# Optimization experiments

Hardware: AMD Instinct MI355X
Metric: run time of the kernel (lower is better)

The kernel has to match this reference:

```python
import jax, jax.numpy as jnp
import numpy as np

EPS = 1e-5

def _ln(x, g, b):
    # layer norm over last dim
    m = jnp.mean(x, axis=-1, keepdims=True)
    v = jnp.mean((x - m) ** 2, axis=-1, keepdims=True)
    return (x - m) * jax.lax.rsqrt(v + EPS) * g + b

def setup_inputs() -> dict:
    key = jax.random.key(0)
    ks = jax.random.split(key, 12)
    B, T, E, H, OUT = 128, 256, 64, 128, 1
    GENOME = 1_000_000
    D = 2 * E  # input_size_lstm
    inp = {}
    inp["indices"] = jax.random.randint(ks[0], (B, T, 2), 0, GENOME, dtype=jnp.int64)
    inp["h0"] = jax.random.normal(ks[1], (B, H), dtype=jnp.float32)
    inp["c0"] = jax.random.normal(ks[2], (B, H), dtype=jnp.float32)
    inp["embed_table"] = jax.random.normal(ks[3], (GENOME, E), dtype=jnp.float32)
    s_ih = 1.0 / np.sqrt(D)
    s_hh = 1.0 / np.sqrt(H)
    inp["W_ih"] = jax.random.uniform(ks[4], (4 * H, D), minval=-s_ih, maxval=s_ih, dtype=jnp.float32)
    inp["W_hh"] = jax.random.uniform(ks[5], (4 * H, H), minval=-s_hh, maxval=s_hh, dtype=jnp.float32)
    inp["g_ih"] = jnp.ones((4 * H,), jnp.float32)
    inp["b_ih"] = jnp.zeros((4 * H,), jnp.float32)
    inp["g_hh"] = jnp.ones((4 * H,), jnp.float32)
    inp["b_hh"] = jnp.zeros((4 * H,), jnp.float32)
    inp["g_c"] = jnp.ones((H,), jnp.float32)
    inp["b_c"] = jnp.zeros((H,), jnp.float32)
    s_o = 1.0 / np.sqrt(H * T)
    inp["W_out"] = jax.random.uniform(ks[6], (OUT * T, H * T), minval=-s_o, maxval=s_o, dtype=jnp.float32)
    inp["b_out"] = jax.random.uniform(ks[7], (OUT * T,), minval=-s_o, maxval=s_o, dtype=jnp.float32)
    return inp

def _forward(indices, embed_table, W_ih, W_hh, g_ih, b_ih, g_hh, b_hh, g_c, b_c, W_out, b_out, h0, c0):
    B, T = indices.shape[0], indices.shape[1]
    H = h0.shape[-1]
    # embedding gather: (B,T,2,E) -> (B,T,2E)
    emb = embed_table[indices].reshape(B, T, -1)
    # precompute input-to-hidden gates for all timesteps: (B,T,4H)
    x_gates = jnp.einsum("btd,gd->btg", emb, W_ih)

    def step(carry, xg):
        h, c = carry
        gates = _ln(xg, g_ih, b_ih) + _ln(h @ W_hh.T, g_hh, b_hh)
        i, f, g, o = jnp.split(gates, 4, axis=-1)
        c_new = jax.nn.sigmoid(f) * c + jax.nn.sigmoid(i) * jnp.tanh(g)
        h_new = jax.nn.sigmoid(o) * jnp.tanh(_ln(c_new, g_c, b_c))
        return (h_new, c_new), h_new

    (_, _), hs = jax.lax.scan(step, (h0, c0), jnp.swapaxes(x_gates, 0, 1))
    # hs: (T,B,H) -> (B,T*H)
    seq_out = jnp.swapaxes(hs, 0, 1).reshape(B, T * H)
    out = jax.nn.sigmoid(seq_out @ W_out.T + b_out)
    return out, emb

def reference(indices, h0, c0, embed_table, W_ih, W_hh, g_ih, b_ih, g_hh, b_hh, g_c, b_c, W_out, b_out):
    return _forward(indices, embed_table, W_ih, W_hh, g_ih, b_ih, g_hh, b_hh, g_c, b_c, W_out, b_out, h0, c0)
```

## Files before the change

kernel.cpp:

```cpp
#include <hip/hip_runtime.h>
#include <cstddef>


typedef __attribute__((ext_vector_type(8))) _Float16 f16x8;
typedef __attribute__((ext_vector_type(4))) float f32x4;

__device__ __forceinline__ float frcp(float x) { return __builtin_amdgcn_rcpf(x); }
__device__ __forceinline__ float sigm(float x) { return frcp(1.0f + __expf(-x)); }
__device__ __forceinline__ float ftanh(float x) {
  float e = __expf(2.0f * x);
  return (e - 1.0f) * frcp(e + 1.0f);
}
__device__ __forceinline__ void split2(float x, unsigned short& hi, unsigned short& lo) {
  _Float16 h = (_Float16)x;
  _Float16 l = (_Float16)((x - (float)h) * 2048.0f);
  hi = *(unsigned short*)&h;
  lo = *(unsigned short*)&l;
}
__device__ __forceinline__ void barrier_lds() {
  asm volatile("s_waitcnt lgkmcnt(0)\n\ts_barrier" ::: "memory");
}

#define SEL4(v, jj) ((jj) == 0 ? (v)[0] : (jj) == 1 ? (v)[1] : (jj) == 2 ? (v)[2] : (v)[3])

__global__ void k_embed(const int* __restrict__ idx, const float4* __restrict__ table4,
                        float4* __restrict__ emb4) {
  int i = blockIdx.x * blockDim.x + threadIdx.x;
  int p = i >> 4, j = i & 15;
  int id = idx[p];
  emb4[(size_t)p * 16 + j] = table4[(size_t)id * 16 + j];
}

__global__ __launch_bounds__(256) void k_gemm_tn(
    const float* __restrict__ A, const float* __restrict__ Bm, float* __restrict__ C,
    int K, int kchunks, int N, size_t partstride)
{
  __shared__ float As[64][65];
  __shared__ float Bs[64][68];
  const int tid = threadIdx.x;
  const int tx = tid & 15, ty = tid >> 4;
  const int m0 = blockIdx.x * 64, n0 = blockIdx.y * 64;
  float acc[4][4] = {};
  size_t kbase = (size_t)blockIdx.z * kchunks * 64;
  for (int kc = 0; kc < kchunks; ++kc) {
    size_t k0 = kbase + (size_t)kc * 64;
    #pragma unroll
    for (int it = 0; it < 4; ++it) {
      int fi = it * 256 + tid;
      int row = fi >> 4, col4 = fi & 15;
      float4 va = *(const float4*)(A + (size_t)(m0 + row) * K + k0 + col4 * 4);
      As[row][col4*4+0] = va.x; As[row][col4*4+1] = va.y;
      As[row][col4*4+2] = va.z; As[row][col4*4+3] = va.w;
      float4 vb = *(const float4*)(Bm + (size_t)(n0 + row) * K + k0 + col4 * 4);
      Bs[col4*4+0][row] = vb.x; Bs[col4*4+1][row] = vb.y;
      Bs[col4*4+2][row] = vb.z; Bs[col4*4+3][row] = vb.w;
    }
    __syncthreads();
    #pragma unroll 8
    for (int k = 0; k < 64; ++k) {
      float a0 = As[ty*4+0][k], a1 = As[ty*4+1][k], a2 = As[ty*4+2][k], a3 = As[ty*4+3][k];
      float b0 = Bs[k][tx*4+0], b1 = Bs[k][tx*4+1], b2 = Bs[k][tx*4+2], b3 = Bs[k][tx*4+3];
      acc[0][0] += a0*b0; acc[0][1] += a0*b1; acc[0][2] += a0*b2; acc[0][3] += a0*b3;
      acc[1][0] += a1*b0; acc[1][1] += a1*b1; acc[1][2] += a1*b2; acc[1][3] += a1*b3;
      acc[2][0] += a2*b0; acc[2][1] += a2*b1; acc[2][2] += a2*b2; acc[2][3] += a2*b3;
      acc[3][0] += a3*b0; acc[3][1] += a3*b1; acc[3][2] += a3*b2; acc[3][3] += a3*b3;
    }
    __syncthreads();
  }
  float* Cp = C + (size_t)blockIdx.z * partstride;
  #pragma unroll
  for (int i = 0; i < 4; ++i) {
    float4 v = make_float4(acc[i][0], acc[i][1], acc[i][2], acc[i][3]);
    *(float4*)(Cp + (size_t)(m0 + ty*4 + i) * N + n0 + tx*4) = v;
  }
}

__global__ __launch_bounds__(256) void k_xln(float4* __restrict__ xg4,
                                             const float4* __restrict__ g4,
                                             const float4* __restrict__ bi4,
                                             const float4* __restrict__ bh4) {
  int row = blockIdx.x * 4 + (threadIdx.x >> 6);
  int lane = threadIdx.x & 63;
  float4* r = xg4 + (size_t)row * 128;
  float4 a = r[lane], b = r[lane + 64];
  float s = a.x + a.y + a.z + a.w + b.x + b.y + b.z + b.w;
  float q = a.x*a.x + a.y*a.y + a.z*a.z + a.w*a.w + b.x*b.x + b.y*b.y + b.z*b.z + b.w*b.w;
  #pragma unroll
  for (int off = 32; off; off >>= 1) { s += __shfl_xor(s, off); q += __shfl_xor(q, off); }
  float m = s * (1.0f / 512.0f);
  float rs = rsqrtf(q * (1.0f / 512.0f) - m * m + 1e-5f);
  float4 ga = g4[lane], gb = g4[64 + lane];
  float4 ia = bi4[lane], ib = bi4[64 + lane];
  float4 ha = bh4[lane], hb = bh4[64 + lane];
  a.x = (a.x - m) * rs * ga.x + ia.x + ha.x; a.y = (a.y - m) * rs * ga.y + ia.y + ha.y;
  a.z = (a.z - m) * rs * ga.z + ia.z + ha.z; a.w = (a.w - m) * rs * ga.w + ia.w + ha.w;
  b.x = (b.x - m) * rs * gb.x + ib.x + hb.x; b.y = (b.y - m) * rs * gb.y + ib.y + hb.y;
  b.z = (b.z - m) * rs * gb.z + ib.z + hb.z; b.w = (b.w - m) * rs * gb.w + ib.w + hb.w;
  r[lane] = a; r[lane + 64] = b;
}

__global__ void k_wprep(const float* __restrict__ Whh, uint4* __restrict__ wfh,
                        uint4* __restrict__ wfl) {
  int i = blockIdx.x * 256 + threadIdx.x;
  int l = i & 63, kc = (i >> 6) & 3, mt = i >> 8;
  int row = mt * 16 + (l & 15);
  int kb = kc * 32 + 8 * (l >> 4);
  float4 a = *(const float4*)(Whh + row * 128 + kb);
  float4 c = *(const float4*)(Whh + row * 128 + kb + 4);
  unsigned short h0,h1,h2,h3,h4,h5,h6,h7, l0,l1,l2,l3,l4,l5,l6,l7;
  split2(a.x,h0,l0); split2(a.y,h1,l1); split2(a.z,h2,l2); split2(a.w,h3,l3);
  split2(c.x,h4,l4); split2(c.y,h5,l5); split2(c.z,h6,l6); split2(c.w,h7,l7);
  uint4 oh, ol;
  oh.x = h0 | ((unsigned)h1 << 16); oh.y = h2 | ((unsigned)h3 << 16);
  oh.z = h4 | ((unsigned)h5 << 16); oh.w = h6 | ((unsigned)h7 << 16);
  ol.x = l0 | ((unsigned)l1 << 16); ol.y = l2 | ((unsigned)l3 << 16);
  ol.z = l4 | ((unsigned)l5 << 16); ol.w = l6 | ((unsigned)l7 << 16);
  wfh[i] = oh; wfl[i] = ol;
}

__global__ __launch_bounds__(512, 2) void k_scan(
    const float* __restrict__ xln,
    const uint4* __restrict__ wfh,
    const uint4* __restrict__ wfl,
    const float* __restrict__ h0, const float* __restrict__ c0,
    const float* __restrict__ g_hh,
    const float* __restrict__ g_c,  const float* __restrict__ b_c,
    float* __restrict__ hs)
{
  const int b = blockIdx.x;
  const int tid = threadIdx.x;
  const int w = tid >> 6, l = tid & 63;
  const int lg = l >> 4;
  const int jj = (l & 15) >> 2;
  const bool wr = (l & 3) == 0;
  const int u = w * 16 + lg * 4 + jj;
  const float inv2048 = 1.0f / 2048.0f;

  __shared__ alignas(16) unsigned short hbh[128];
  __shared__ alignas(16) unsigned short hbl[128];
  __shared__ float2 hred[8];
  __shared__ float2 cred[8];

  uint4 afh0[4], afh1[4], afh2[4], afh3[4];
  uint4 afl0[4], afl1[4], afl2[4], afl3[4];
  #pragma unroll
  for (int kc = 0; kc < 4; ++kc) {
    afh0[kc] = wfh[((w     ) * 4 + kc) * 64 + l];
    afh1[kc] = wfh[((w +  8) * 4 + kc) * 64 + l];
    afh2[kc] = wfh[((w + 16) * 4 + kc) * 64 + l];
    afh3[kc] = wfh[((w + 24) * 4 + kc) * 64 + l];
    afl0[kc] = wfl[((w     ) * 4 + kc) * 64 + l];
    afl1[kc] = wfl[((w +  8) * 4 + kc) * 64 + l];
    afl2[kc] = wfl[((w + 16) * 4 + kc) * 64 + l];
    afl3[kc] = wfl[((w + 24) * 4 + kc) * 64 + l];
  }
  #pragma unroll
  for (int kc = 0; kc < 4; ++kc) {
    asm volatile("" : "+v"(afh0[kc].x), "+v"(afh0[kc].y), "+v"(afh0[kc].z), "+v"(afh0[kc].w));
    asm volatile("" : "+v"(afh1[kc].x), "+v"(afh1[kc].y), "+v"(afh1[kc].z), "+v"(afh1[kc].w));
    asm volatile("" : "+v"(afh2[kc].x), "+v"(afh2[kc].y), "+v"(afh2[kc].z), "+v"(afh2[kc].w));
    asm volatile("" : "+v"(afh3[kc].x), "+v"(afh3[kc].y), "+v"(afh3[kc].z), "+v"(afh3[kc].w));
    asm volatile("" : "+v"(afl0[kc].x), "+v"(afl0[kc].y), "+v"(afl0[kc].z), "+v"(afl0[kc].w));
    asm volatile("" : "+v"(afl1[kc].x), "+v"(afl1[kc].y), "+v"(afl1[kc].z), "+v"(afl1[kc].w));
    asm volatile("" : "+v"(afl2[kc].x), "+v"(afl2[kc].y), "+v"(afl2[kc].z), "+v"(afl2[kc].w));
    asm volatile("" : "+v"(afl3[kc].x), "+v"(afl3[kc].y), "+v"(afl3[kc].z), "+v"(afl3[kc].w));
  }

  const float ghI = g_hh[u], ghF = g_hh[128 + u], ghG = g_hh[256 + u], ghO = g_hh[384 + u];
  const float gcv = g_c[u], bcv = b_c[u];
  float cv = c0[b * 128 + u];
  if (wr) {
    unsigned short hi, lo;
    split2(h0[b * 128 + u], hi, lo);
    hbh[u] = hi; hbl[u] = lo;
  }
  __syncthreads();

  const float* xgb = xln + (size_t)b * 256 * 512;
  float* hsb = hs + (size_t)b * 256 * 128;

  float xI = xgb[u], xF = xgb[128 + u], xG = xgb[256 + u], xO = xgb[384 + u];

  for (int t = 0; t < 256; ++t) {
    const float* xn = xgb + (((t + 1) & 255) << 9);
    float nI = xn[u], nF = xn[128 + u], nG = xn[256 + u], nO = xn[384 + u];

    f32x4 acc0 = {0,0,0,0}, acc1 = {0,0,0,0}, acc2 = {0,0,0,0}, acc3 = {0,0,0,0};
    f32x4 e0 = {0,0,0,0}, e1 = {0,0,0,0}, e2 = {0,0,0,0}, e3 = {0,0,0,0};
    #pragma unroll
    for (int kc = 0; kc < 4; ++kc) {
      uint4 buh = *(const uint4*)((const char*)hbh + kc * 64 + 16 * lg);
      uint4 bul = *(const uint4*)((const char*)hbl + kc * 64 + 16 * lg);
      f16x8 bh = *(f16x8*)&buh;
      f16x8 bl = *(f16x8*)&bul;
      acc0 = __builtin_amdgcn_mfma_f32_16x16x32_f16(*(f16x8*)&afh0[kc], bh, acc0, 0, 0, 0);
      acc1 = __builtin_amdgcn_mfma_f32_16x16x32_f16(*(f16x8*)&afh1[kc], bh, acc1, 0, 0, 0);
      acc2 = __builtin_amdgcn_mfma_f32_16x16x32_f16(*(f16x8*)&afh2[kc], bh, acc2, 0, 0, 0);
      acc3 = __builtin_amdgcn_mfma_f32_16x16x32_f16(*(f16x8*)&afh3[kc], bh, acc3, 0, 0, 0);
      e0 = __builtin_amdgcn_mfma_f32_16x16x32_f16(*(f16x8*)&afh0[kc], bl, e0, 0, 0, 0);
      e1 = __builtin_amdgcn_mfma_f32_16x16x32_f16(*(f16x8*)&afh1[kc], bl, e1, 0, 0, 0);
      e2 = __builtin_amdgcn_mfma_f32_16x16x32_f16(*(f16x8*)&afh2[kc], bl, e2, 0, 0, 0);
      e3 = __builtin_amdgcn_mfma_f32_16x16x32_f16(*(f16x8*)&afh3[kc], bl, e3, 0, 0, 0);
      e0 = __builtin_amdgcn_mfma_f32_16x16x32_f16(*(f16x8*)&afl0[kc], bh, e0, 0, 0, 0);
      e1 = __builtin_amdgcn_mfma_f32_16x16x32_f16(*(f16x8*)&afl1[kc], bh, e1, 0, 0, 0);
      e2 = __builtin_amdgcn_mfma_f32_16x16x32_f16(*(f16x8*)&afl2[kc], bh, e2, 0, 0, 0);
      e3 = __builtin_amdgcn_mfma_f32_16x16x32_f16(*(f16x8*)&afl3[kc], bh, e3, 0, 0, 0);
    }
    f32x4 a0, a1, a2, a3;
    #pragma unroll
    for (int j = 0; j < 4; ++j) {
      a0[j] = acc0[j] + e0[j] * inv2048;
      a1[j] = acc1[j] + e1[j] * inv2048;
      a2[j] = acc2[j] + e2[j] * inv2048;
      a3[j] = acc3[j] + e3[j] * inv2048;
    }

    float s = 0.f, q = 0.f;
    #pragma unroll
    for (int j = 0; j < 4; ++j) {
      s += a0[j] + a1[j] + a2[j] + a3[j];
      q += a0[j]*a0[j] + a1[j]*a1[j] + a2[j]*a2[j] + a3[j]*a3[j];
    }
    s += __shfl_xor(s, 16); s += __shfl_xor(s, 32);
    q += __shfl_xor(q, 16); q += __shfl_xor(q, 32);
    if (l == 0) hred[w] = make_float2(s, q);

    barrier_lds();

    float rsx = 0.f, rsq = 0.f;
    #pragma unroll
    for (int i = 0; i < 8; ++i) { float2 v = hred[i]; rsx += v.x; rsq += v.y; }
    float mh = rsx * (1.0f / 512.0f);
    float rh = rsqrtf(rsq * (1.0f / 512.0f) - mh * mh + 1e-5f);

    float aI = SEL4(a0, jj), aF = SEL4(a1, jj), aG = SEL4(a2, jj), aO = SEL4(a3, jj);
    float gI = xI + (aI - mh) * rh * ghI;
    float gF = xF + (aF - mh) * rh * ghF;
    float gG = xG + (aG - mh) * rh * ghG;
    float gO = xO + (aO - mh) * rh * ghO;

    float cn = sigm(gF) * cv + sigm(gI) * ftanh(gG);
    cv = cn;

    float cs = cn, cq = cn * cn;
    #pragma unroll
    for (int off = 32; off; off >>= 1) { cs += __shfl_xor(cs, off); cq += __shfl_xor(cq, off); }
    if (l == 0) cred[w] = make_float2(cs, cq);

    barrier_lds();

    float tcs = 0.f, tcq = 0.f;
    #pragma unroll
    for (int i = 0; i < 8; ++i) { float2 v = cred[i]; tcs += v.x; tcq += v.y; }
    float mc = tcs * (1.0f / 512.0f);
    float rc = rsqrtf(tcq * (1.0f / 512.0f) - mc * mc + 1e-5f);

    float lnc = (cn - mc) * rc * gcv + bcv;
    float hn = sigm(gO) * ftanh(lnc);

    if (wr) {
      unsigned short hi, lo;
      split2(hn, hi, lo);
      hbh[u] = hi; hbl[u] = lo;
      hsb[(size_t)t * 128 + u] = hn;
    }
    xI = nI; xF = nF; xG = nG; xO = nO;

    barrier_lds();
  }
}

__global__ void k_reduce(const float* __restrict__ part, const float* __restrict__ b_out,
                         float* __restrict__ out) {
  int i = blockIdx.x * 256 + threadIdx.x;
  float s = b_out[i & 255];
  #pragma unroll
  for (int z = 0; z < 32; ++z) s += part[(size_t)z * 32768 + i];
  out[i] = sigm(s);
}

extern "C" void kernel_launch(void* const* d_in, const int* in_sizes, int n_in,
                              void* d_out, int out_size, void* d_ws, size_t ws_size,
                              hipStream_t stream) {
  const int*   idx   = (const int*)  d_in[0];
  const float* h0    = (const float*)d_in[1];
  const float* c0    = (const float*)d_in[2];
  const float* table = (const float*)d_in[3];
  const float* W_ih  = (const float*)d_in[4];
  const float* W_hh  = (const float*)d_in[5];
  const float* g_ih  = (const float*)d_in[6];
  const float* b_ih  = (const float*)d_in[7];
  const float* g_hh  = (const float*)d_in[8];
  const float* b_hh  = (const float*)d_in[9];
  const float* g_c   = (const float*)d_in[10];
  const float* b_c   = (const float*)d_in[11];
  const float* W_out = (const float*)d_in[12];
  const float* b_out = (const float*)d_in[13];

  float* out  = (float*)d_out;
  float* emb  = out + 32768;
  float* ws   = (float*)d_ws;
  float* xg   = ws;
  float* hsb  = ws + 16777216;
  uint4* wfh  = (uint4*)(ws + 20971520);
  uint4* wfl  = (uint4*)(ws + 21004288);
  float* part = ws + 21037056;

  k_embed<<<4096, 256, 0, stream>>>(idx, (const float4*)table, (float4*)emb);
  k_gemm_tn<<<dim3(512, 8, 1), 256, 0, stream>>>(emb, W_ih, xg, 128, 2, 512, 0);
  k_xln<<<8192, 256, 0, stream>>>((float4*)xg, (const float4*)g_ih,
                                  (const float4*)b_ih, (const float4*)b_hh);
  k_wprep<<<32, 256, 0, stream>>>(W_hh, wfh, wfl);
  k_scan<<<128, 512, 0, stream>>>(xg, wfh, wfl, h0, c0, g_hh, g_c, b_c, hsb);
  k_gemm_tn<<<dim3(2, 4, 32), 256, 0, stream>>>(hsb, W_out, part, 32768, 16, 256, 32768);
  k_reduce<<<128, 256, 0, stream>>>(part, b_out, out);
}
```

Baseline: 649.4 us.

## Warp-specialize LSTM scan and ping-pong two sequences per block

The recurrent scan kernel now runs two batch rows per 1024-thread block. Eight waves do only the MFMA matrix-vector product with W_hh, and eight waves do the layer norms and gate math. The two sequences alternate, so one sequence's matvec overlaps the other's elementwise step, with results passed through double-buffered LDS. Wave reductions now use DPP instead of shuffles, and the MFMA section runs at raised priority. In exchange, half as many CUs are used, the gate waves compute redundantly, and launch_bounds(1024,4) may force a tight register budget and spill the register-resident weights.

```diff
diff --git a/kernel.cpp b/kernel.cpp
--- a/kernel.cpp
+++ b/kernel.cpp
@@ -21,7 +21,17 @@
   asm volatile("s_waitcnt lgkmcnt(0)\n\ts_barrier" ::: "memory");
 }
 
-#define SEL4(v, jj) ((jj) == 0 ? (v)[0] : (jj) == 1 ? (v)[1] : (jj) == 2 ? (v)[2] : (v)[3])
+#define DPP_ADD(x, ctrl, rmask)                                                     \
+  __int_as_float(__builtin_amdgcn_update_dpp(0, __float_as_int(x), ctrl, rmask, 0xf, true))
+__device__ __forceinline__ float wave_sum(float x) {
+  x += DPP_ADD(x, 0x111, 0xf);
+  x += DPP_ADD(x, 0x112, 0xf);
+  x += DPP_ADD(x, 0x114, 0xf);
+  x += DPP_ADD(x, 0x118, 0xf);
+  x += DPP_ADD(x, 0x142, 0xa);
+  x += DPP_ADD(x, 0x143, 0xc);
+  return __int_as_float(__builtin_amdgcn_readlane(__float_as_int(x), 63));
+}
 
 __global__ void k_embed(const int* __restrict__ idx, const float4* __restrict__ table4,
                         float4* __restrict__ emb4) {
@@ -118,7 +128,7 @@
   wfh[i] = oh; wfl[i] = ol;
 }
 
-__global__ __launch_bounds__(512, 2) void k_scan(
+__global__ __launch_bounds__(1024, 4) void k_scan(
     const float* __restrict__ xln,
     const uint4* __restrict__ wfh,
     const uint4* __restrict__ wfl,
@@ -127,146 +137,182 @@
     const float* __restrict__ g_c,  const float* __restrict__ b_c,
     float* __restrict__ hs)
 {
-  const int b = blockIdx.x;
+  const int bid = blockIdx.x;
   const int tid = threadIdx.x;
   const int w = tid >> 6, l = tid & 63;
   const int lg = l >> 4;
-  const int jj = (l & 15) >> 2;
-  const bool wr = (l & 3) == 0;
-  const int u = w * 16 + lg * 4 + jj;
   const float inv2048 = 1.0f / 2048.0f;
 
-  __shared__ alignas(16) unsigned short hbh[128];
-  __shared__ alignas(16) unsigned short hbl[128];
-  __shared__ float2 hred[8];
-  __shared__ float2 cred[8];
-
-  uint4 afh0[4], afh1[4], afh2[4], afh3[4];
-  uint4 afl0[4], afl1[4], afl2[4], afl3[4];
-  #pragma unroll
-  for (int kc = 0; kc < 4; ++kc) {
-    afh0[kc] = wfh[((w     ) * 4 + kc) * 64 + l];
-    afh1[kc] = wfh[((w +  8) * 4 + kc) * 64 + l];
-    afh2[kc] = wfh[((w + 16) * 4 + kc) * 64 + l];
-    afh3[kc] = wfh[((w + 24) * 4 + kc) * 64 + l];
-    afl0[kc] = wfl[((w     ) * 4 + kc) * 64 + l];
-    afl1[kc] = wfl[((w +  8) * 4 + kc) * 64 + l];
-    afl2[kc] = wfl[((w + 16) * 4 + kc) * 64 + l];
-    afl3[kc] = wfl[((w + 24) * 4 + kc) * 64 + l];
-  }
-  #pragma unroll
-  for (int kc = 0; kc < 4; ++kc) {
-    asm volatile("" : "+v"(afh0[kc].x), "+v"(afh0[kc].y), "+v"(afh0[kc].z), "+v"(afh0[kc].w));
-    asm volatile("" : "+v"(afh1[kc].x), "+v"(afh1[kc].y), "+v"(afh1[kc].z), "+v"(afh1[kc].w));
-    asm volatile("" : "+v"(afh2[kc].x), "+v"(afh2[kc].y), "+v"(afh2[kc].z), "+v"(afh2[kc].w));
-    asm volatile("" : "+v"(afh3[kc].x), "+v"(afh3[kc].y), "+v"(afh3[kc].z), "+v"(afh3[kc].w));
-    asm volatile("" : "+v"(afl0[kc].x), "+v"(afl0[kc].y), "+v"(afl0[kc].z), "+v"(afl0[kc].w));
-    asm volatile("" : "+v"(afl1[kc].x), "+v"(afl1[kc].y), "+v"(afl1[kc].z), "+v"(afl1[kc].w));
-    asm volatile("" : "+v"(afl2[kc].x), "+v"(afl2[kc].y), "+v"(afl2[kc].z), "+v"(afl2[kc].w));
-    asm volatile("" : "+v"(afl3[kc].x), "+v"(afl3[kc].y), "+v"(afl3[kc].z), "+v"(afl3[kc].w));
-  }
-
-  const float ghI = g_hh[u], ghF = g_hh[128 + u], ghG = g_hh[256 + u], ghO = g_hh[384 + u];
-  const float gcv = g_c[u], bcv = b_c[u];
-  float cv = c0[b * 128 + u];
-  if (wr) {
+  __shared__ alignas(16) unsigned short hbh[2][128];
+  __shared__ alignas(16) unsigned short hbl[2][128];
+  __shared__ alignas(16) float accL[2][512];
+  __shared__ alignas(16) float2 hred[2][8];
+
+  const int bA = bid * 2, bB = bid * 2 + 1;
+
+  if (tid < 128) {
     unsigned short hi, lo;
-    split2(h0[b * 128 + u], hi, lo);
-    hbh[u] = hi; hbl[u] = lo;
+    split2(h0[bA * 128 + tid], hi, lo); hbh[0][tid] = hi; hbl[0][tid] = lo;
+    split2(h0[bB * 128 + tid], hi, lo); hbh[1][tid] = hi; hbl[1][tid] = lo;
   }
   __syncthreads();
 
-  const float* xgb = xln + (size_t)b * 256 * 512;
-  float* hsb = hs + (size_t)b * 256 * 128;
-
-  float xI = xgb[u], xF = xgb[128 + u], xG = xgb[256 + u], xO = xgb[384 + u];
-
-  for (int t = 0; t < 256; ++t) {
-    const float* xn = xgb + (((t + 1) & 255) << 9);
-    float nI = xn[u], nF = xn[128 + u], nG = xn[256 + u], nO = xn[384 + u];
-
-    f32x4 acc0 = {0,0,0,0}, acc1 = {0,0,0,0}, acc2 = {0,0,0,0}, acc3 = {0,0,0,0};
-    f32x4 e0 = {0,0,0,0}, e1 = {0,0,0,0}, e2 = {0,0,0,0}, e3 = {0,0,0,0};
+  if (w < 8) {
+    const int mw = w;
+    uint4 afh0[4], afh1[4], afh2[4], afh3[4];
+    uint4 afl0[4], afl1[4], afl2[4], afl3[4];
     #pragma unroll
     for (int kc = 0; kc < 4; ++kc) {
-      uint4 buh = *(const uint4*)((const char*)hbh + kc * 64 + 16 * lg);
-      uint4 bul = *(const uint4*)((const char*)hbl + kc * 64 + 16 * lg);
-      f16x8 bh = *(f16x8*)&buh;
-      f16x8 bl = *(f16x8*)&bul;
-      acc0 = __builtin_amdgcn_mfma_f32_16x16x32_f16(*(f16x8*)&afh0[kc], bh, acc0, 0, 0, 0);
-      acc1 = __builtin_amdgcn_mfma_f32_16x16x32_f16(*(f16x8*)&afh1[kc], bh, acc1, 0, 0, 0);
-      acc2 = __builtin_amdgcn_mfma_f32_16x16x32_f16(*(f16x8*)&afh2[kc], bh, acc2, 0, 0, 0);
-      acc3 = __builtin_amdgcn_mfma_f32_16x16x32_f16(*(f16x8*)&afh3[kc], bh, acc3, 0, 0, 0);
-      e0 = __builtin_amdgcn_mfma_f32_16x16x32_f16(*(f16x8*)&afh0[kc], bl, e0, 0, 0, 0);
-      e1 = __builtin_amdgcn_mfma_f32_16x16x32_f16(*(f16x8*)&afh1[kc], bl, e1, 0, 0, 0);
-      e2 = __builtin_amdgcn_mfma_f32_16x16x32_f16(*(f16x8*)&afh2[kc], bl, e2, 0, 0, 0);
-      e3 = __builtin_amdgcn_mfma_f32_16x16x32_f16(*(f16x8*)&afh3[kc], bl, e3, 0, 0, 0);
-      e0 = __builtin_amdgcn_mfma_f32_16x16x32_f16(*(f16x8*)&afl0[kc], bh, e0, 0, 0, 0);
-      e1 = __builtin_amdgcn_mfma_f32_16x16x32_f16(*(f16x8*)&afl1[kc], bh, e1, 0, 0, 0);
-      e2 = __builtin_amdgcn_mfma_f32_16x16x32_f16(*(f16x8*)&afl2[kc], bh, e2, 0, 0, 0);
-      e3 = __builtin_amdgcn_mfma_f32_16x16x32_f16(*(f16x8*)&afl3[kc], bh, e3, 0, 0, 0);
-    }
-    f32x4 a0, a1, a2, a3;
+      afh0[kc] = wfh[((mw     ) * 4 + kc) * 64 + l];
+      afh1[kc] = wfh[((mw +  8) * 4 + kc) * 64 + l];
+      afh2[kc] = wfh[((mw + 16) * 4 + kc) * 64 + l];
+      afh3[kc] = wfh[((mw + 24) * 4 + kc) * 64 + l];
+      afl0[kc] = wfl[((mw     ) * 4 + kc) * 64 + l];
+      afl1[kc] = wfl[((mw +  8) * 4 + kc) * 64 + l];
+      afl2[kc] = wfl[((mw + 16) * 4 + kc) * 64 + l];
+      afl3[kc] = wfl[((mw + 24) * 4 + kc) * 64 + l];
+    }
     #pragma unroll
-    for (int j = 0; j < 4; ++j) {
-      a0[j] = acc0[j] + e0[j] * inv2048;
-      a1[j] = acc1[j] + e1[j] * inv2048;
-      a2[j] = acc2[j] + e2[j] * inv2048;
-      a3[j] = acc3[j] + e3[j] * inv2048;
-    }
-
-    float s = 0.f, q = 0.f;
-    #pragma unroll
-    for (int j = 0; j < 4; ++j) {
-      s += a0[j] + a1[j] + a2[j] + a3[j];
-      q += a0[j]*a0[j] + a1[j]*a1[j] + a2[j]*a2[j] + a3[j]*a3[j];
-    }
-    s += __shfl_xor(s, 16); s += __shfl_xor(s, 32);
-    q += __shfl_xor(q, 16); q += __shfl_xor(q, 32);
-    if (l == 0) hred[w] = make_float2(s, q);
-
+    for (int kc = 0; kc < 4; ++kc) {
+      asm volatile("" : "+v"(afh0[kc].x), "+v"(afh0[kc].y), "+v"(afh0[kc].z), "+v"(afh0[kc].w));
+      asm volatile("" : "+v"(afh1[kc].x), "+v"(afh1[kc].y), "+v"(afh1[kc].z), "+v"(afh1[kc].w));
+      asm volatile("" : "+v"(afh2[kc].x), "+v"(afh2[kc].y), "+v"(afh2[kc].z), "+v"(afh2[kc].w));
+      asm volatile("" : "+v"(afh3[kc].x), "+v"(afh3[kc].y), "+v"(afh3[kc].z), "+v"(afh3[kc].w));
+      asm volatile("" : "+v"(afl0[kc].x), "+v"(afl0[kc].y), "+v"(afl0[kc].z), "+v"(afl0[kc].w));
+      asm volatile("" : "+v"(afl1[kc].x), "+v"(afl1[kc].y), "+v"(afl1[kc].z), "+v"(afl1[kc].w));
+      asm volatile("" : "+v"(afl2[kc].x), "+v"(afl2[kc].y), "+v"(afl2[kc].z), "+v"(afl2[kc].w));
+      asm volatile("" : "+v"(afl3[kc].x), "+v"(afl3[kc].y), "+v"(afl3[kc].z), "+v"(afl3[kc].w));
+    }
+
+    auto MVSTEP = [&](int r) {
+      const char* Hh = (const char*)hbh[r];
+      const char* Hl = (const char*)hbl[r];
+      f32x4 acc0 = {0,0,0,0}, acc1 = {0,0,0,0}, acc2 = {0,0,0,0}, acc3 = {0,0,0,0};
+      f32x4 e0 = {0,0,0,0}, e1 = {0,0,0,0}, e2 = {0,0,0,0}, e3 = {0,0,0,0};
+      __builtin_amdgcn_s_setprio(1);
+      #pragma unroll
+      for (int kc = 0; kc < 4; ++kc) {
+        uint4 buh = *(const uint4*)(Hh + kc * 64 + 16 * lg);
+        uint4 bul = *(const uint4*)(Hl + kc * 64 + 16 * lg);
+        f16x8 bh = *(f16x8*)&buh;
+        f16x8 bl = *(f16x8*)&bul;
+        acc0 = __builtin_amdgcn_mfma_f32_16x16x32_f16(*(f16x8*)&afh0[kc], bh, acc0, 0, 0, 0);
+        acc1 = __builtin_amdgcn_mfma_f32_16x16x32_f16(*(f16x8*)&afh1[kc], bh, acc1, 0, 0, 0);
+        acc2 = __builtin_amdgcn_mfma_f32_16x16x32_f16(*(f16x8*)&afh2[kc], bh, acc2, 0, 0, 0);
+        acc3 = __builtin_amdgcn_mfma_f32_16x16x32_f16(*(f16x8*)&afh3[kc], bh, acc3, 0, 0, 0);
+        e0 = __builtin_amdgcn_mfma_f32_16x16x32_f16(*(f16x8*)&afh0[kc], bl, e0, 0, 0, 0);
+        e1 = __builtin_amdgcn_mfma_f32_16x16x32_f16(*(f16x8*)&afh1[kc], bl, e1, 0, 0, 0);
+        e2 = __builtin_amdgcn_mfma_f32_16x16x32_f16(*(f16x8*)&afh2[kc], bl, e2, 0, 0, 0);
+        e3 = __builtin_amdgcn_mfma_f32_16x16x32_f16(*(f16x8*)&afh3[kc], bl, e3, 0, 0, 0);
+        e0 = __builtin_amdgcn_mfma_f32_16x16x32_f16(*(f16x8*)&afl0[kc], bh, e0, 0, 0, 0);
+        e1 = __builtin_amdgcn_mfma_f32_16x16x32_f16(*(f16x8*)&afl1[kc], bh, e1, 0, 0, 0);
+        e2 = __builtin_amdgcn_mfma_f32_16x16x32_f16(*(f16x8*)&afl2[kc], bh, e2, 0, 0, 0);
+        e3 = __builtin_amdgcn_mfma_f32_16x16x32_f16(*(f16x8*)&afl3[kc], bh, e3, 0, 0, 0);
+      }
+      __builtin_amdgcn_s_setprio(0);
+      f32x4 a0, a1, a2, a3;
+      #pragma unroll
+      for (int j = 0; j < 4; ++j) {
+        a0[j] = acc0[j] + e0[j] * inv2048;
+        a1[j] = acc1[j] + e1[j] * inv2048;
+        a2[j] = acc2[j] + e2[j] * inv2048;
+        a3[j] = acc3[j] + e3[j] * inv2048;
+      }
+      float s = 0.f, q = 0.f;
+      #pragma unroll
+      for (int j = 0; j < 4; ++j) {
+        s += a0[j] + a1[j] + a2[j] + a3[j];
+        q += a0[j]*a0[j] + a1[j]*a1[j] + a2[j]*a2[j] + a3[j]*a3[j];
+      }
+      s = wave_sum(s); q = wave_sum(q);
+      if (l == 0) hred[r][mw] = make_float2(s, q);
+      if ((l & 15) == 0) {
+        float* ap = &accL[r][0];
+        *(f32x4*)(ap + (mw     ) * 16 + lg * 4) = a0;
+        *(f32x4*)(ap + (mw +  8) * 16 + lg * 4) = a1;
+        *(f32x4*)(ap + (mw + 16) * 16 + lg * 4) = a2;
+        *(f32x4*)(ap + (mw + 24) * 16 + lg * 4) = a3;
+      }
+    };
+
+    MVSTEP(0); barrier_lds();
+    MVSTEP(1); barrier_lds();
+    for (int k = 1; k < 256; ++k) {
+      MVSTEP(0); barrier_lds();
+      MVSTEP(1); barrier_lds();
+    }
     barrier_lds();
-
-    float rsx = 0.f, rsq = 0.f;
-    #pragma unroll
-    for (int i = 0; i < 8; ++i) { float2 v = hred[i]; rsx += v.x; rsq += v.y; }
-    float mh = rsx * (1.0f / 512.0f);
-    float rh = rsqrtf(rsq * (1.0f / 512.0f) - mh * mh + 1e-5f);
-
-    float aI = SEL4(a0, jj), aF = SEL4(a1, jj), aG = SEL4(a2, jj), aO = SEL4(a3, jj);
-    float gI = xI + (aI - mh) * rh * ghI;
-    float gF = xF + (aF - mh) * rh * ghF;
-    float gG = xG + (aG - mh) * rh * ghG;
-    float gO = xO + (aO - mh) * rh * ghO;
-
-    float cn = sigm(gF) * cv + sigm(gI) * ftanh(gG);
-    cv = cn;
-
-    float cs = cn, cq = cn * cn;
-    #pragma unroll
-    for (int off = 32; off; off >>= 1) { cs += __shfl_xor(cs, off); cq += __shfl_xor(cq, off); }
-    if (l == 0) cred[w] = make_float2(cs, cq);
+  } else {
+    const int u0 = 2 * l;
+    float2 ghI = *(const float2*)(g_hh + u0);
+    float2 ghF = *(const float2*)(g_hh + 128 + u0);
+    float2 ghG = *(const float2*)(g_hh + 256 + u0);
+    float2 ghO = *(const float2*)(g_hh + 384 + u0);
+    float2 gc2 = *(const float2*)(g_c + u0);
+    float2 bc2 = *(const float2*)(b_c + u0);
+    float cvA0 = c0[bA * 128 + u0], cvA1 = c0[bA * 128 + u0 + 1];
+    float cvB0 = c0[bB * 128 + u0], cvB1 = c0[bB * 128 + u0 + 1];
+    const float* xgA = xln + (size_t)bA * 131072;
+    const float* xgB = xln + (size_t)bB * 131072;
+    float* hsA = hs + (size_t)bA * 32768;
+    float* hsB = hs + (size_t)bB * 32768;
+    float2 xAI = *(const float2*)(xgA + u0),        xAF = *(const float2*)(xgA + 128 + u0);
+    float2 xAG = *(const float2*)(xgA + 256 + u0),  xAO = *(const float2*)(xgA + 384 + u0);
+    float2 xBI = *(const float2*)(xgB + u0),        xBF = *(const float2*)(xgB + 128 + u0);
+    float2 xBG = *(const float2*)(xgB + 256 + u0),  xBO = *(const float2*)(xgB + 384 + u0);
+
+    auto GTSTEP = [&](int r, int k, float2& xI, float2& xF, float2& xG, float2& xO,
+                      float& cv0, float& cv1, const float* xg, float* hsr) {
+      const float4* hp = (const float4*)&hred[r][0];
+      float4 p0 = hp[0], p1 = hp[1], p2 = hp[2], p3 = hp[3];
+      float rsx = ((p0.x + p0.z) + (p1.x + p1.z)) + ((p2.x + p2.z) + (p3.x + p3.z));
+      float rsq = ((p0.y + p0.w) + (p1.y + p1.w)) + ((p2.y + p2.w) + (p3.y + p3.w));
+      float mh = rsx * (1.0f / 8192.0f);
+      float rh = rsqrtf(rsq * (1.0f / 8192.0f) - mh * mh + 1e-5f);
+
+      const float* ar = &accL[r][0];
+      float2 aI = *(const float2*)(ar + u0);
+      float2 aF = *(const float2*)(ar + 128 + u0);
+      float2 aG = *(const float2*)(ar + 256 + u0);
+      float2 aO = *(const float2*)(ar + 384 + u0);
+
+      float gI0 = xI.x + (aI.x - mh) * rh * ghI.x, gI1 = xI.y + (aI.y - mh) * rh * ghI.y;
+      float gF0 = xF.x + (aF.x - mh) * rh * ghF.x, gF1 = xF.y + (aF.y - mh) * rh * ghF.y;
+      float gG0 = xG.x + (aG.x - mh) * rh * ghG.x, gG1 = xG.y + (aG.y - mh) * rh * ghG.y;
+      float gO0 = xO.x + (aO.x - mh) * rh * ghO.x, gO1 = xO.y + (aO.y - mh) * rh * ghO.y;
+
+      const float* xn = xg + (size_t)((k + 1) & 255) * 512;
+      xI = *(const float2*)(xn + u0);       xF = *(const float2*)(xn + 128 + u0);
+      xG = *(const float2*)(xn + 256 + u0); xO = *(const float2*)(xn + 384 + u0);
+
+      float cn0 = sigm(gF0) * cv0 + sigm(gI0) * ftanh(gG0);
+      float cn1 = sigm(gF1) * cv1 + sigm(gI1) * ftanh(gG1);
+      cv0 = cn0; cv1 = cn1;
+
+      float tcs = wave_sum(cn0 + cn1);
+      float tcq = wave_sum(cn0 * cn0 + cn1 * cn1);
+      float mc = tcs * (1.0f / 128.0f);
+      float rc = rsqrtf(tcq * (1.0f / 128.0f) - mc * mc + 1e-5f);
+
+      float hn0 = sigm(gO0) * ftanh((cn0 - mc) * rc * gc2.x + bc2.x);
+      float hn1 = sigm(gO1) * ftanh((cn1 - mc) * rc * gc2.y + bc2.y);
+
+      if (w == 8) {
+        unsigned short h0a, l0a, h1a, l1a;
+        split2(hn0, h0a, l0a); split2(hn1, h1a, l1a);
+        *(unsigned int*)((char*)hbh[r] + 4 * l) = (unsigned)h0a | ((unsigned)h1a << 16);
+        *(unsigned int*)((char*)hbl[r] + 4 * l) = (unsigned)l0a | ((unsigned)l1a << 16);
+        *(float2*)(hsr + (size_t)k * 128 + u0) = make_float2(hn0, hn1);
+      }
+    };
 
     barrier_lds();
-
-    float tcs = 0.f, tcq = 0.f;
-    #pragma unroll
-    for (int i = 0; i < 8; ++i) { float2 v = cred[i]; tcs += v.x; tcq += v.y; }
-    float mc = tcs * (1.0f / 512.0f);
-    float rc = rsqrtf(tcq * (1.0f / 512.0f) - mc * mc + 1e-5f);
-
-    float lnc = (cn - mc) * rc * gcv + bcv;
-    float hn = sigm(gO) * ftanh(lnc);
-
-    if (wr) {
-      unsigned short hi, lo;
-      split2(hn, hi, lo);
-      hbh[u] = hi; hbl[u] = lo;
-      hsb[(size_t)t * 128 + u] = hn;
-    }
-    xI = nI; xF = nF; xG = nG; xO = nO;
-
-    barrier_lds();
+    GTSTEP(0, 0, xAI, xAF, xAG, xAO, cvA0, cvA1, xgA, hsA); barrier_lds();
+    for (int k = 1; k < 256; ++k) {
+      GTSTEP(1, k - 1, xBI, xBF, xBG, xBO, cvB0, cvB1, xgB, hsB); barrier_lds();
+      GTSTEP(0, k,     xAI, xAF, xAG, xAO, cvA0, cvA1, xgA, hsA); barrier_lds();
+    }
+    GTSTEP(1, 255, xBI, xBF, xBG, xBO, cvB0, cvB1, xgB, hsB); barrier_lds();
   }
 }
 
@@ -311,7 +357,7 @@
   k_xln<<<8192, 256, 0, stream>>>((float4*)xg, (const float4*)g_ih,
                                   (const float4*)b_ih, (const float4*)b_hh);
   k_wprep<<<32, 256, 0, stream>>>(W_hh, wfh, wfl);
-  k_scan<<<128, 512, 0, stream>>>(xg, wfh, wfl, h0, c0, g_hh, g_c, b_c, hsb);
+  k_scan<<<64, 1024, 0, stream>>>(xg, wfh, wfl, h0, c0, g_hh, g_c, b_c, hsb);
   k_gemm_tn<<<dim3(2, 4, 32), 256, 0, stream>>>(hsb, W_out, part, 32768, 16, 256, 32768);
   k_reduce<<<128, 256, 0, stream>>>(part, b_out, out);
 }
```

Result: slower. 1.964 ms (+202.4%).

## Replicate cell update per wave to drop two barriers per LSTM step

Applied to the files above, without the earlier changes.

The scan step previously needed three block barriers: one for the hidden-gate layernorm stats, one for the cell-state layernorm stats, and one to publish h. Now each wave writes its MFMA accumulators to double-buffered LDS. After a single barrier, every wave redundantly computes all 128 cell units (two per lane) using a DPP wave reduction for the cell layernorm, then writes h into its own private LDS copy. This trades redundant elementwise math and transcendentals (8x replicated) for fewer barriers on the sequential critical path.

```diff
diff --git a/kernel.cpp b/kernel.cpp
--- a/kernel.cpp
+++ b/kernel.cpp
@@ -21,7 +21,17 @@
   asm volatile("s_waitcnt lgkmcnt(0)\n\ts_barrier" ::: "memory");
 }
 
-#define SEL4(v, jj) ((jj) == 0 ? (v)[0] : (jj) == 1 ? (v)[1] : (jj) == 2 ? (v)[2] : (v)[3])
+#define DPP_ADD(x, ctrl, rmask)                                                     \
+  __int_as_float(__builtin_amdgcn_update_dpp(0, __float_as_int(x), ctrl, rmask, 0xf, true))
+__device__ __forceinline__ float wave_sum(float x) {
+  x += DPP_ADD(x, 0x111, 0xf);
+  x += DPP_ADD(x, 0x112, 0xf);
+  x += DPP_ADD(x, 0x114, 0xf);
+  x += DPP_ADD(x, 0x118, 0xf);
+  x += DPP_ADD(x, 0x142, 0xa);
+  x += DPP_ADD(x, 0x143, 0xc);
+  return __int_as_float(__builtin_amdgcn_readlane(__float_as_int(x), 63));
+}
 
 __global__ void k_embed(const int* __restrict__ idx, const float4* __restrict__ table4,
                         float4* __restrict__ emb4) {
@@ -131,15 +141,13 @@
   const int tid = threadIdx.x;
   const int w = tid >> 6, l = tid & 63;
   const int lg = l >> 4;
-  const int jj = (l & 15) >> 2;
-  const bool wr = (l & 3) == 0;
-  const int u = w * 16 + lg * 4 + jj;
+  const int u0 = 2 * l;
   const float inv2048 = 1.0f / 2048.0f;
 
-  __shared__ alignas(16) unsigned short hbh[128];
-  __shared__ alignas(16) unsigned short hbl[128];
-  __shared__ float2 hred[8];
-  __shared__ float2 cred[8];
+  __shared__ alignas(16) unsigned short hwh[8][128];
+  __shared__ alignas(16) unsigned short hwl[8][128];
+  __shared__ alignas(16) float accL[2][512];
+  __shared__ alignas(16) float2 hred[2][8];
 
   uint4 afh0[4], afh1[4], afh2[4], afh3[4];
   uint4 afl0[4], afl1[4], afl2[4], afl3[4];
@@ -166,31 +174,41 @@
     asm volatile("" : "+v"(afl3[kc].x), "+v"(afl3[kc].y), "+v"(afl3[kc].z), "+v"(afl3[kc].w));
   }
 
-  const float ghI = g_hh[u], ghF = g_hh[128 + u], ghG = g_hh[256 + u], ghO = g_hh[384 + u];
-  const float gcv = g_c[u], bcv = b_c[u];
-  float cv = c0[b * 128 + u];
-  if (wr) {
-    unsigned short hi, lo;
-    split2(h0[b * 128 + u], hi, lo);
-    hbh[u] = hi; hbl[u] = lo;
+  const float2 ghI = *(const float2*)(g_hh + u0);
+  const float2 ghF = *(const float2*)(g_hh + 128 + u0);
+  const float2 ghG = *(const float2*)(g_hh + 256 + u0);
+  const float2 ghO = *(const float2*)(g_hh + 384 + u0);
+  const float2 gc2 = *(const float2*)(g_c + u0);
+  const float2 bc2 = *(const float2*)(b_c + u0);
+  float cv0 = c0[b * 128 + u0], cv1 = c0[b * 128 + u0 + 1];
+
+  {
+    float2 h2 = *(const float2*)(h0 + b * 128 + u0);
+    unsigned short a_, b_, c_, d_;
+    split2(h2.x, a_, b_); split2(h2.y, c_, d_);
+    *(unsigned int*)&hwh[w][u0] = (unsigned)a_ | ((unsigned)c_ << 16);
+    *(unsigned int*)&hwl[w][u0] = (unsigned)b_ | ((unsigned)d_ << 16);
   }
   __syncthreads();
 
-  const float* xgb = xln + (size_t)b * 256 * 512;
-  float* hsb = hs + (size_t)b * 256 * 128;
-
-  float xI = xgb[u], xF = xgb[128 + u], xG = xgb[256 + u], xO = xgb[384 + u];
-
+  const float* xgb = xln + (size_t)b * 131072;
+  float* hsb = hs + (size_t)b * 32768;
+
+  float2 xI = *(const float2*)(xgb + u0);
+  float2 xF = *(const float2*)(xgb + 128 + u0);
+  float2 xG = *(const float2*)(xgb + 256 + u0);
+  float2 xO = *(const float2*)(xgb + 384 + u0);
+
+  int buf = 0;
   for (int t = 0; t < 256; ++t) {
-    const float* xn = xgb + (((t + 1) & 255) << 9);
-    float nI = xn[u], nF = xn[128 + u], nG = xn[256 + u], nO = xn[384 + u];
-
+    const char* Hh = (const char*)&hwh[w][0];
+    const char* Hl = (const char*)&hwl[w][0];
     f32x4 acc0 = {0,0,0,0}, acc1 = {0,0,0,0}, acc2 = {0,0,0,0}, acc3 = {0,0,0,0};
     f32x4 e0 = {0,0,0,0}, e1 = {0,0,0,0}, e2 = {0,0,0,0}, e3 = {0,0,0,0};
     #pragma unroll
     for (int kc = 0; kc < 4; ++kc) {
-      uint4 buh = *(const uint4*)((const char*)hbh + kc * 64 + 16 * lg);
-      uint4 bul = *(const uint4*)((const char*)hbl + kc * 64 + 16 * lg);
+      uint4 buh = *(const uint4*)(Hh + kc * 64 + 16 * lg);
+      uint4 bul = *(const uint4*)(Hl + kc * 64 + 16 * lg);
       f16x8 bh = *(f16x8*)&buh;
       f16x8 bl = *(f16x8*)&bul;
       acc0 = __builtin_amdgcn_mfma_f32_16x16x32_f16(*(f16x8*)&afh0[kc], bh, acc0, 0, 0, 0);
@@ -223,50 +241,62 @@
     }
     s += __shfl_xor(s, 16); s += __shfl_xor(s, 32);
     q += __shfl_xor(q, 16); q += __shfl_xor(q, 32);
-    if (l == 0) hred[w] = make_float2(s, q);
+    if (l == 0) hred[buf][w] = make_float2(s, q);
+    if ((l & 15) == 0) {
+      float* ap = &accL[buf][0];
+      *(f32x4*)(ap + (w     ) * 16 + lg * 4) = a0;
+      *(f32x4*)(ap + (w +  8) * 16 + lg * 4) = a1;
+      *(f32x4*)(ap + (w + 16) * 16 + lg * 4) = a2;
+      *(f32x4*)(ap + (w + 24) * 16 + lg * 4) = a3;
+    }
 
     barrier_lds();
 
-    float rsx = 0.f, rsq = 0.f;
-    #pragma unroll
-    for (int i = 0; i < 8; ++i) { float2 v = hred[i]; rsx += v.x; rsq += v.y; }
+    const float4* hp = (const float4*)&hred[buf][0];
+    float4 p0 = hp[0], p1 = hp[1], p2 = hp[2], p3 = hp[3];
+    float rsx = ((p0.x + p0.z) + (p1.x + p1.z)) + ((p2.x + p2.z) + (p3.x + p3.z));
+    float rsq = ((p0.y + p0.w) + (p1.y + p1.w)) + ((p2.y + p2.w) + (p3.y + p3.w));
     float mh = rsx * (1.0f / 512.0f);
     float rh = rsqrtf(rsq * (1.0f / 512.0f) - mh * mh + 1e-5f);
 
-    float aI = SEL4(a0, jj), aF = SEL4(a1, jj), aG = SEL4(a2, jj), aO = SEL4(a3, jj);
-    float gI = xI + (aI - mh) * rh * ghI;
-    float gF = xF + (aF - mh) * rh * ghF;
-    float gG = xG + (aG - mh) * rh * ghG;
-    float gO = xO + (aO - mh) * rh * ghO;
-
-    float cn = sigm(gF) * cv + sigm(gI) * ftanh(gG);
-    cv = cn;
-
-    float cs = cn, cq = cn * cn;
-    #pragma unroll
-    for (int off = 32; off; off >>= 1) { cs += __shfl_xor(cs, off); cq += __shfl_xor(cq, off); }
-    if (l == 0) cred[w] = make_float2(cs, cq);
-
-    barrier_lds();
-
-    float tcs = 0.f, tcq = 0.f;
-    #pragma unroll
-    for (int i = 0; i < 8; ++i) { float2 v = cred[i]; tcs += v.x; tcq += v.y; }
-    float mc = tcs * (1.0f / 512.0f);
-    float rc = rsqrtf(tcq * (1.0f / 512.0f) - mc * mc + 1e-5f);
-
-    float lnc = (cn - mc) * rc * gcv + bcv;
-    float hn = sigm(gO) * ftanh(lnc);
-
-    if (wr) {
-      unsigned short hi, lo;
-      split2(hn, hi, lo);
-      hbh[u] = hi; hbl[u] = lo;
-      hsb[(size_t)t * 128 + u] = hn;
-    }
-    xI = nI; xF = nF; xG = nG; xO = nO;
-
-    barrier_lds();
+    const float* ar = &accL[buf][0];
+    float2 aI = *(const float2*)(ar + u0);
+    float2 aF = *(const float2*)(ar + 128 + u0);
+    float2 aG = *(const float2*)(ar + 256 + u0);
+    float2 aO = *(const float2*)(ar + 384 + u0);
+
+    float gI0 = xI.x + (aI.x - mh) * rh * ghI.x, gI1 = xI.y + (aI.y - mh) * rh * ghI.y;
+    float gF0 = xF.x + (aF.x - mh) * rh * ghF.x, gF1 = xF.y + (aF.y - mh) * rh * ghF.y;
+    float gG0 = xG.x + (aG.x - mh) * rh * ghG.x, gG1 = xG.y + (aG.y - mh) * rh * ghG.y;
+    float gO0 = xO.x + (aO.x - mh) * rh * ghO.x, gO1 = xO.y + (aO.y - mh) * rh * ghO.y;
+
+    const float* xn = xgb + (size_t)(((t + 1) & 255)) * 512;
+    xI = *(const float2*)(xn + u0);
+    xF = *(const float2*)(xn + 128 + u0);
+    xG = *(const float2*)(xn + 256 + u0);
+    xO = *(const float2*)(xn + 384 + u0);
+
+    float cn0 = sigm(gF0) * cv0 + sigm(gI0) * ftanh(gG0);
+    float cn1 = sigm(gF1) * cv1 + sigm(gI1) * ftanh(gG1);
+    cv0 = cn0; cv1 = cn1;
+
+    float tcs = wave_sum(cn0 + cn1);
+    float tcq = wave_sum(cn0 * cn0 + cn1 * cn1);
+    float mc = tcs * (1.0f / 128.0f);
+    float rc = rsqrtf(tcq * (1.0f / 128.0f) - mc * mc + 1e-5f);
+
+    float hn0 = sigm(gO0) * ftanh((cn0 - mc) * rc * gc2.x + bc2.x);
+    float hn1 = sigm(gO1) * ftanh((cn1 - mc) * rc * gc2.y + bc2.y);
+
+    {
+      unsigned short a_, b_, c_, d_;
+      split2(hn0, a_, b_); split2(hn1, c_, d_);
+      *(unsigned int*)&hwh[w][u0] = (unsigned)a_ | ((unsigned)c_ << 16);
+      *(unsigned int*)&hwl[w][u0] = (unsigned)b_ | ((unsigned)d_ << 16);
+    }
+    if (w == 0) *(float2*)(hsb + (size_t)t * 128 + u0) = make_float2(hn0, hn1);
+
+    buf ^= 1;
   }
 }
 
```

Result: slower. 672.7 us (+3.6%).
